# Performance work log

Hardware: AMD Instinct MI355X
Metric: run time of the kernel (lower is better)

The kernel has to match this reference:

```python
import jax, jax.numpy as jnp
import numpy as np

LABEL_SMOOTHING = 0.1
K_SLOPE = 5.0
N, D = 8192, 256


def setup_inputs() -> dict:
    key = jax.random.key(0)
    k1, k2, k3 = jax.random.split(key, 3)
    return {
        "image_features1": jax.random.normal(k1, (N, D), dtype=jnp.float32),
        "image_features2": jax.random.normal(k2, (N, D), dtype=jnp.float32),
        "logit_scale": jnp.asarray(14.2857, dtype=jnp.float32),  # ~ 1/0.07 CLIP temp
        "positive_weights": jax.random.normal(k3, (N,), dtype=jnp.float32),
    }


def _l2_normalize(x, axis=-1, eps=1e-12):
    # matches F.normalize(dim=-1)
    norm = jnp.linalg.norm(x, axis=axis, keepdims=True)
    return x / jnp.maximum(norm, eps)


def _weighted_infonce(sim, eps):
    # per row i: (1-eps_i)*(-sim[i,i] + lse_i) + eps_i*(-mean(sim[i,:]) + lse_i)
    #          = lse_i - (1-eps_i)*sim[i,i] - eps_i*mean_i
    n = sim.shape[0]
    lse = jax.nn.logsumexp(sim, axis=1)            # [n]
    diag = jnp.diagonal(sim)                       # [n]
    row_mean = jnp.mean(sim, axis=1)               # [n]
    per_row = lse - (1.0 - eps) * diag - eps * row_mean
    return jnp.sum(per_row) / n


def reference(image_features1, image_features2, logit_scale, positive_weights):
    f1 = _l2_normalize(image_features1)
    f2 = _l2_normalize(image_features2)
    logits12 = logit_scale * (f1 @ f2.T)           # [N, N]
    # eps = 1 - (1 - label_smoothing) * sigmoid(k * w)
    eps = 1.0 - (1.0 - LABEL_SMOOTHING) * jax.nn.sigmoid(K_SLOPE * positive_weights)
    loss1 = _weighted_infonce(logits12, eps)
    loss2 = _weighted_infonce(logits12.T, eps)
    return (loss1 + loss2) / 2.0
```

## Files before the change

kernel.cpp:

```cpp
#include <hip/hip_runtime.h>
#include <hip/hip_bf16.h>

#define NN 8192
#define DD 256
#define LOG2E 1.4426950408889634f
#define LN2f 0.6931471805599453f

typedef __attribute__((ext_vector_type(8))) short short8;
typedef __attribute__((ext_vector_type(4))) float f32x4;

__device__ __forceinline__ unsigned short f2bf(float x) {
    unsigned int u = __float_as_uint(x);
    u += 0x7fff + ((u >> 16) & 1);
    return (unsigned short)(u >> 16);
}
__device__ __forceinline__ float epsf(float w) {
    return 1.f - 0.9f / (1.f + __expf(-5.f * w));
}

__global__ __launch_bounds__(256) void nrm_kernel(
    const float* __restrict__ f1, const float* __restrict__ f2,
    const float* __restrict__ scale_p, const float* __restrict__ wts,
    unsigned short* __restrict__ f1n, unsigned short* __restrict__ f2n,
    float* __restrict__ diag, float* __restrict__ rse, float* __restrict__ cse,
    float* __restrict__ S1p, float* __restrict__ S2p,
    float* __restrict__ T1p, float* __restrict__ T2p)
{
    __shared__ float4 red[4][256];
    const int w = threadIdx.x >> 6, lane = threadIdx.x & 63;
    const int row = blockIdx.x * 4 + w;
    const float4 a = reinterpret_cast<const float4*>(f1 + (size_t)row * DD)[lane];
    const float4 b = reinterpret_cast<const float4*>(f2 + (size_t)row * DD)[lane];
    float sa = a.x * a.x + a.y * a.y + a.z * a.z + a.w * a.w;
    float sb = b.x * b.x + b.y * b.y + b.z * b.z + b.w * b.w;
    float sab = a.x * b.x + a.y * b.y + a.z * b.z + a.w * b.w;
#pragma unroll
    for (int off = 1; off < 64; off <<= 1) {
        sa += __shfl_xor(sa, off);
        sb += __shfl_xor(sb, off);
        sab += __shfl_xor(sab, off);
    }
    const float s = scale_p[0];
    const float n1 = fmaxf(sqrtf(sa), 1e-12f);
    const float n2 = fmaxf(sqrtf(sb), 1e-12f);
    const float e = epsf(wts[row]);
    if (lane == 0) { diag[row] = s * sab / (n1 * n2); rse[row] = 0.f; cse[row] = 0.f; }
    const float r1 = s * LOG2E / n1, r2 = 1.0f / n2;
    const float v0 = a.x * r1, v1 = a.y * r1, v2 = a.z * r1, v3 = a.w * r1;
    const float u0 = b.x * r2, u1 = b.y * r2, u2 = b.z * r2, u3 = b.w * r2;
    ushort4 o1, o2;
    o1.x = f2bf(v0); o1.y = f2bf(v1); o1.z = f2bf(v2); o1.w = f2bf(v3);
    o2.x = f2bf(u0); o2.y = f2bf(u1); o2.z = f2bf(u2); o2.w = f2bf(u3);
    reinterpret_cast<ushort4*>(f1n + (size_t)row * DD)[lane] = o1;
    reinterpret_cast<ushort4*>(f2n + (size_t)row * DD)[lane] = o2;
    red[w][lane * 4 + 0] = make_float4(v0, e * v0, u0, e * u0);
    red[w][lane * 4 + 1] = make_float4(v1, e * v1, u1, e * u1);
    red[w][lane * 4 + 2] = make_float4(v2, e * v2, u2, e * u2);
    red[w][lane * 4 + 3] = make_float4(v3, e * v3, u3, e * u3);
    __syncthreads();
    const int c = threadIdx.x;
    const int part = (blockIdx.x & 63) * 256 + c;
    const float4 q0 = red[0][c], q1 = red[1][c], q2 = red[2][c], q3 = red[3][c];
    atomicAdd(&S1p[part], q0.x + q1.x + q2.x + q3.x);
    atomicAdd(&T1p[part], q0.y + q1.y + q2.y + q3.y);
    atomicAdd(&S2p[part], q0.z + q1.z + q2.z + q3.z);
    atomicAdd(&T2p[part], q0.w + q1.w + q2.w + q3.w);
}

__global__ __launch_bounds__(256, 2) void gemm_kernel(
    const unsigned short* __restrict__ f1n, const unsigned short* __restrict__ f2n,
    float* __restrict__ rowsumexp, float* __restrict__ colsumexp)
{
    __shared__ char Bs[2][64 * 512];
    __shared__ float colbuf[2][1024];
    const int bid = blockIdx.x;
    const int bm = bid >> 3, bc = bid & 7;
    const int w = threadIdx.x >> 6, lane = threadIdx.x & 63;
    const int wr = (w >> 1) * 64, wc = (w & 1) * 32;
    const int lhi = lane >> 4, llo = lane & 15;

    const char* aBase = (const char*)f1n + ((size_t)(bm * 128 + wr + llo) * 512) + lhi * 16;
    short8 av[4][8];
#pragma unroll
    for (int m = 0; m < 4; ++m)
#pragma unroll
        for (int ks = 0; ks < 8; ++ks)
            av[m][ks] = *(const short8*)(aBase + (size_t)(m * 16) * 512 + ks * 64);
#pragma unroll
    for (int m = 0; m < 4; ++m)
#pragma unroll
        for (int ks = 0; ks < 8; ++ks)
            asm volatile("" : "+v"(av[m][ks]));

    const char* bBase = (const char*)f2n + (size_t)bc * 1024 * 512;

    auto stage = [&](int buf, int tile) {
#pragma unroll
        for (int i = 0; i < 8; ++i) {
            const int r = w * 16 + i * 2 + (lane >> 5);
            const int cs = (lane & 31) ^ (r & 15);
            __builtin_amdgcn_global_load_lds(
                (const __attribute__((address_space(1))) unsigned int*)
                    (bBase + (size_t)(tile * 64 + r) * 512 + cs * 16),
                (__attribute__((address_space(3))) unsigned int*)
                    (&Bs[buf][(w * 16 + i * 2) * 512]), 16, 0, 0);
        }
    };

    float rowpart[16];
#pragma unroll
    for (int i = 0; i < 16; ++i) rowpart[i] = 0.f;

    stage(0, 0);

    const int rb0 = wc + llo, rb1 = wc + 16 + llo;
    const int sw = llo << 4;

    for (int t = 0; t < 16; ++t) {
        const int cur = t & 1;
        if (t < 15) {
            stage(cur ^ 1, t + 1);
            asm volatile("s_waitcnt vmcnt(8)" ::: "memory");
        } else {
            asm volatile("s_waitcnt vmcnt(0)" ::: "memory");
        }
        __builtin_amdgcn_s_barrier();
        __builtin_amdgcn_sched_barrier(0);

        f32x4 acc[4][2];
#pragma unroll
        for (int m = 0; m < 4; ++m) {
            acc[m][0] = (f32x4){0.f, 0.f, 0.f, 0.f};
            acc[m][1] = (f32x4){0.f, 0.f, 0.f, 0.f};
        }
        const char* bs = Bs[cur];
#pragma unroll
        for (int ks = 0; ks < 8; ++ks) {
            const int kb = ks * 64 + lhi * 16;
            const short8 bv0 = *(const short8*)(bs + rb0 * 512 + (kb ^ sw));
            const short8 bv1 = *(const short8*)(bs + rb1 * 512 + (kb ^ sw));
#pragma unroll
            for (int m = 0; m < 4; ++m) {
                acc[m][0] = __builtin_amdgcn_mfma_f32_16x16x32_bf16(av[m][ks], bv0, acc[m][0], 0, 0, 0);
                acc[m][1] = __builtin_amdgcn_mfma_f32_16x16x32_bf16(av[m][ks], bv1, acc[m][1], 0, 0, 0);
            }
        }

        float cee0 = 0.f, cee1 = 0.f;
#pragma unroll
        for (int m = 0; m < 4; ++m)
#pragma unroll
            for (int j = 0; j < 4; ++j) {
                const float e0 = __builtin_exp2f(acc[m][0][j]);
                const float e1 = __builtin_exp2f(acc[m][1][j]);
                rowpart[m * 4 + j] += e0 + e1;
                cee0 += e0; cee1 += e1;
            }
        cee0 += __shfl_xor(cee0, 16); cee0 += __shfl_xor(cee0, 32);
        cee1 += __shfl_xor(cee1, 16); cee1 += __shfl_xor(cee1, 32);
        if (lhi == 0) {
            colbuf[w >> 1][t * 64 + wc + llo] = cee0;
            colbuf[w >> 1][t * 64 + wc + 16 + llo] = cee1;
        }
        __builtin_amdgcn_s_barrier();
    }

    __syncthreads();

#pragma unroll
    for (int m = 0; m < 4; ++m)
#pragma unroll
        for (int j = 0; j < 4; ++j) {
            float v = rowpart[m * 4 + j];
            v += __shfl_xor(v, 1); v += __shfl_xor(v, 2);
            v += __shfl_xor(v, 4); v += __shfl_xor(v, 8);
            if (llo == 0)
                atomicAdd(&rowsumexp[bm * 128 + wr + m * 16 + lhi * 4 + j], v);
        }
    for (int c = threadIdx.x; c < 1024; c += 256)
        atomicAdd(&colsumexp[bc * 1024 + c], colbuf[0][c] + colbuf[1][c]);
}

__global__ __launch_bounds__(256) void finA_kernel(
    const float* __restrict__ rse, const float* __restrict__ cse,
    const float* __restrict__ diag, const float* __restrict__ wts,
    float* __restrict__ totalp)
{
    const int i = blockIdx.x * 256 + threadIdx.x;
    const float eps = epsf(wts[i]);
    float a = __logf(rse[i]) + __logf(cse[i]) - 2.f * (1.f - eps) * diag[i];
#pragma unroll
    for (int off = 1; off < 64; off <<= 1) a += __shfl_xor(a, off);
    __shared__ float red[4];
    if ((threadIdx.x & 63) == 0) red[threadIdx.x >> 6] = a;
    __syncthreads();
    if (threadIdx.x == 0)
        atomicAdd(totalp, red[0] + red[1] + red[2] + red[3]);
}

__global__ __launch_bounds__(1024) void finB_kernel(
    const float* __restrict__ S1p, const float* __restrict__ S2p,
    const float* __restrict__ T1p, const float* __restrict__ T2p,
    const float* __restrict__ totalp, float* __restrict__ out)
{
    const int t = threadIdx.x;
    __shared__ float4 pr4[4][256];
    {
        const int col = t & 255, seg = t >> 8;
        float s1 = 0.f, t1 = 0.f, s2 = 0.f, t2 = 0.f;
#pragma unroll
        for (int q = 0; q < 16; ++q) {
            const int idx = (seg * 16 + q) * 256 + col;
            s1 += S1p[idx]; t1 += T1p[idx]; s2 += S2p[idx]; t2 += T2p[idx];
        }
        pr4[seg][col] = make_float4(s1, t1, s2, t2);
    }
    __syncthreads();
    float a = 0.f;
    if (t < 256) {
        const float4 q0 = pr4[0][t], q1 = pr4[1][t], q2 = pr4[2][t], q3 = pr4[3][t];
        const float s1 = q0.x + q1.x + q2.x + q3.x;
        const float t1 = q0.y + q1.y + q2.y + q3.y;
        const float s2 = q0.z + q1.z + q2.z + q3.z;
        const float t2 = q0.w + q1.w + q2.w + q3.w;
        a = (t1 * s2 + s1 * t2) * (LN2f / (float)NN);
    }
#pragma unroll
    for (int off = 1; off < 64; off <<= 1) a += __shfl_xor(a, off);
    __shared__ float red[16];
    if ((t & 63) == 0) red[t >> 6] = a;
    __syncthreads();
    if (t == 0) {
        float dot = 0.f;
#pragma unroll
        for (int i = 0; i < 16; ++i) dot += red[i];
        out[0] = (totalp[0] - dot) * (1.f / (2.f * (float)NN));
    }
}

extern "C" void kernel_launch(void* const* d_in, const int* in_sizes, int n_in,
                              void* d_out, int out_size, void* d_ws, size_t ws_size,
                              hipStream_t stream) {
    (void)in_sizes; (void)n_in; (void)out_size; (void)ws_size;
    const float* f1 = (const float*)d_in[0];
    const float* f2 = (const float*)d_in[1];
    const float* scale = (const float*)d_in[2];
    const float* wts = (const float*)d_in[3];
    float* out = (float*)d_out;

    char* ws = (char*)d_ws;
    unsigned short* f1n = (unsigned short*)ws;
    unsigned short* f2n = (unsigned short*)(ws + (size_t)4 * 1024 * 1024);
    float* fb = (float*)(ws + (size_t)8 * 1024 * 1024);
    float* rse  = fb;
    float* cse  = fb + 8192;
    float* diag = fb + 16384;
    float* S1p  = fb + 24576;
    float* S2p  = fb + 24576 + 16384;
    float* T1p  = fb + 24576 + 32768;
    float* T2p  = fb + 24576 + 49152;
    float* totalp = fb + 24576 + 65536;

    hipMemsetAsync(S1p, 0, ((size_t)4 * 16384 + 16) * sizeof(float), stream);
    nrm_kernel<<<NN / 4, 256, 0, stream>>>(f1, f2, scale, wts, f1n, f2n,
                                           diag, rse, cse, S1p, S2p, T1p, T2p);
    gemm_kernel<<<512, 256, 0, stream>>>(f1n, f2n, rse, cse);
    finA_kernel<<<32, 256, 0, stream>>>(rse, cse, diag, wts, totalp);
    finB_kernel<<<1, 1024, 0, stream>>>(S1p, S2p, T1p, T2p, totalp, out);
}
```

Measured before the change: 77.08 us.

## Replace atomic column-sum partials with per-block stores and hierarchical reduction

```diff
diff --git a/kernel.cpp b/kernel.cpp
--- a/kernel.cpp
+++ b/kernel.cpp
@@ -23,48 +23,56 @@
     const float* __restrict__ scale_p, const float* __restrict__ wts,
     unsigned short* __restrict__ f1n, unsigned short* __restrict__ f2n,
     float* __restrict__ diag, float* __restrict__ rse, float* __restrict__ cse,
-    float* __restrict__ S1p, float* __restrict__ S2p,
-    float* __restrict__ T1p, float* __restrict__ T2p)
+    float4* __restrict__ STp, float* __restrict__ totalp)
 {
     __shared__ float4 red[4][256];
     const int w = threadIdx.x >> 6, lane = threadIdx.x & 63;
-    const int row = blockIdx.x * 4 + w;
-    const float4 a = reinterpret_cast<const float4*>(f1 + (size_t)row * DD)[lane];
-    const float4 b = reinterpret_cast<const float4*>(f2 + (size_t)row * DD)[lane];
-    float sa = a.x * a.x + a.y * a.y + a.z * a.z + a.w * a.w;
-    float sb = b.x * b.x + b.y * b.y + b.z * b.z + b.w * b.w;
-    float sab = a.x * b.x + a.y * b.y + a.z * b.z + a.w * b.w;
-#pragma unroll
-    for (int off = 1; off < 64; off <<= 1) {
-        sa += __shfl_xor(sa, off);
-        sb += __shfl_xor(sb, off);
-        sab += __shfl_xor(sab, off);
-    }
     const float s = scale_p[0];
-    const float n1 = fmaxf(sqrtf(sa), 1e-12f);
-    const float n2 = fmaxf(sqrtf(sb), 1e-12f);
-    const float e = epsf(wts[row]);
-    if (lane == 0) { diag[row] = s * sab / (n1 * n2); rse[row] = 0.f; cse[row] = 0.f; }
-    const float r1 = s * LOG2E / n1, r2 = 1.0f / n2;
-    const float v0 = a.x * r1, v1 = a.y * r1, v2 = a.z * r1, v3 = a.w * r1;
-    const float u0 = b.x * r2, u1 = b.y * r2, u2 = b.z * r2, u3 = b.w * r2;
-    ushort4 o1, o2;
-    o1.x = f2bf(v0); o1.y = f2bf(v1); o1.z = f2bf(v2); o1.w = f2bf(v3);
-    o2.x = f2bf(u0); o2.y = f2bf(u1); o2.z = f2bf(u2); o2.w = f2bf(u3);
-    reinterpret_cast<ushort4*>(f1n + (size_t)row * DD)[lane] = o1;
-    reinterpret_cast<ushort4*>(f2n + (size_t)row * DD)[lane] = o2;
-    red[w][lane * 4 + 0] = make_float4(v0, e * v0, u0, e * u0);
-    red[w][lane * 4 + 1] = make_float4(v1, e * v1, u1, e * u1);
-    red[w][lane * 4 + 2] = make_float4(v2, e * v2, u2, e * u2);
-    red[w][lane * 4 + 3] = make_float4(v3, e * v3, u3, e * u3);
+    const int row0 = blockIdx.x * 16 + w * 4;
+    float s1a[4] = {0,0,0,0}, t1a[4] = {0,0,0,0};
+    float s2a[4] = {0,0,0,0}, t2a[4] = {0,0,0,0};
+#pragma unroll
+    for (int r = 0; r < 4; ++r) {
+        const int row = row0 + r;
+        const float4 a = reinterpret_cast<const float4*>(f1 + (size_t)row * DD)[lane];
+        const float4 b = reinterpret_cast<const float4*>(f2 + (size_t)row * DD)[lane];
+        float sa = a.x * a.x + a.y * a.y + a.z * a.z + a.w * a.w;
+        float sb = b.x * b.x + b.y * b.y + b.z * b.z + b.w * b.w;
+        float sab = a.x * b.x + a.y * b.y + a.z * b.z + a.w * b.w;
+#pragma unroll
+        for (int off = 1; off < 64; off <<= 1) {
+            sa += __shfl_xor(sa, off);
+            sb += __shfl_xor(sb, off);
+            sab += __shfl_xor(sab, off);
+        }
+        const float n1 = fmaxf(sqrtf(sa), 1e-12f);
+        const float n2 = fmaxf(sqrtf(sb), 1e-12f);
+        const float e = epsf(wts[row]);
+        if (lane == 0) { diag[row] = s * sab / (n1 * n2); rse[row] = 0.f; cse[row] = 0.f; }
+        const float r1 = s * LOG2E / n1, r2 = 1.0f / n2;
+        const float v0 = a.x * r1, v1 = a.y * r1, v2 = a.z * r1, v3 = a.w * r1;
+        const float u0 = b.x * r2, u1 = b.y * r2, u2 = b.z * r2, u3 = b.w * r2;
+        ushort4 o1, o2;
+        o1.x = f2bf(v0); o1.y = f2bf(v1); o1.z = f2bf(v2); o1.w = f2bf(v3);
+        o2.x = f2bf(u0); o2.y = f2bf(u1); o2.z = f2bf(u2); o2.w = f2bf(u3);
+        reinterpret_cast<ushort4*>(f1n + (size_t)row * DD)[lane] = o1;
+        reinterpret_cast<ushort4*>(f2n + (size_t)row * DD)[lane] = o2;
+        s1a[0] += v0; s1a[1] += v1; s1a[2] += v2; s1a[3] += v3;
+        t1a[0] += e * v0; t1a[1] += e * v1; t1a[2] += e * v2; t1a[3] += e * v3;
+        s2a[0] += u0; s2a[1] += u1; s2a[2] += u2; s2a[3] += u3;
+        t2a[0] += e * u0; t2a[1] += e * u1; t2a[2] += e * u2; t2a[3] += e * u3;
+    }
+#pragma unroll
+    for (int k = 0; k < 4; ++k)
+        red[w][lane * 4 + k] = make_float4(s1a[k], t1a[k], s2a[k], t2a[k]);
     __syncthreads();
     const int c = threadIdx.x;
-    const int part = (blockIdx.x & 63) * 256 + c;
     const float4 q0 = red[0][c], q1 = red[1][c], q2 = red[2][c], q3 = red[3][c];
-    atomicAdd(&S1p[part], q0.x + q1.x + q2.x + q3.x);
-    atomicAdd(&T1p[part], q0.y + q1.y + q2.y + q3.y);
-    atomicAdd(&S2p[part], q0.z + q1.z + q2.z + q3.z);
-    atomicAdd(&T2p[part], q0.w + q1.w + q2.w + q3.w);
+    STp[blockIdx.x * 256 + c] = make_float4(q0.x + q1.x + q2.x + q3.x,
+                                            q0.y + q1.y + q2.y + q3.y,
+                                            q0.z + q1.z + q2.z + q3.z,
+                                            q0.w + q1.w + q2.w + q3.w);
+    if (blockIdx.x == 0 && threadIdx.x == 0) totalp[0] = 0.f;
 }
 
 __global__ __launch_bounds__(256, 2) void gemm_kernel(
@@ -184,56 +192,49 @@
 __global__ __launch_bounds__(256) void finA_kernel(
     const float* __restrict__ rse, const float* __restrict__ cse,
     const float* __restrict__ diag, const float* __restrict__ wts,
+    const float4* __restrict__ STp, float4* __restrict__ P2,
     float* __restrict__ totalp)
 {
-    const int i = blockIdx.x * 256 + threadIdx.x;
+    const int g = blockIdx.x, t = threadIdx.x;
+    const int i = g * 256 + t;
     const float eps = epsf(wts[i]);
     float a = __logf(rse[i]) + __logf(cse[i]) - 2.f * (1.f - eps) * diag[i];
 #pragma unroll
     for (int off = 1; off < 64; off <<= 1) a += __shfl_xor(a, off);
     __shared__ float red[4];
-    if ((threadIdx.x & 63) == 0) red[threadIdx.x >> 6] = a;
-    __syncthreads();
-    if (threadIdx.x == 0)
-        atomicAdd(totalp, red[0] + red[1] + red[2] + red[3]);
-}
-
-__global__ __launch_bounds__(1024) void finB_kernel(
-    const float* __restrict__ S1p, const float* __restrict__ S2p,
-    const float* __restrict__ T1p, const float* __restrict__ T2p,
-    const float* __restrict__ totalp, float* __restrict__ out)
+    if ((t & 63) == 0) red[t >> 6] = a;
+
+    float4 s = make_float4(0.f, 0.f, 0.f, 0.f);
+#pragma unroll 4
+    for (int j = 0; j < 16; ++j) {
+        const float4 v = STp[(g * 16 + j) * 256 + t];
+        s.x += v.x; s.y += v.y; s.z += v.z; s.w += v.w;
+    }
+    P2[g * 256 + t] = s;
+
+    __syncthreads();
+    if (t == 0) atomicAdd(totalp, red[0] + red[1] + red[2] + red[3]);
+}
+
+__global__ __launch_bounds__(256) void fin_kernel(
+    const float4* __restrict__ P2, const float* __restrict__ totalp,
+    float* __restrict__ out)
 {
     const int t = threadIdx.x;
-    __shared__ float4 pr4[4][256];
-    {
-        const int col = t & 255, seg = t >> 8;
-        float s1 = 0.f, t1 = 0.f, s2 = 0.f, t2 = 0.f;
-#pragma unroll
-        for (int q = 0; q < 16; ++q) {
-            const int idx = (seg * 16 + q) * 256 + col;
-            s1 += S1p[idx]; t1 += T1p[idx]; s2 += S2p[idx]; t2 += T2p[idx];
-        }
-        pr4[seg][col] = make_float4(s1, t1, s2, t2);
-    }
-    __syncthreads();
-    float a = 0.f;
-    if (t < 256) {
-        const float4 q0 = pr4[0][t], q1 = pr4[1][t], q2 = pr4[2][t], q3 = pr4[3][t];
-        const float s1 = q0.x + q1.x + q2.x + q3.x;
-        const float t1 = q0.y + q1.y + q2.y + q3.y;
-        const float s2 = q0.z + q1.z + q2.z + q3.z;
-        const float t2 = q0.w + q1.w + q2.w + q3.w;
-        a = (t1 * s2 + s1 * t2) * (LN2f / (float)NN);
-    }
-#pragma unroll
-    for (int off = 1; off < 64; off <<= 1) a += __shfl_xor(a, off);
-    __shared__ float red[16];
-    if ((t & 63) == 0) red[t >> 6] = a;
+    float4 s = make_float4(0.f, 0.f, 0.f, 0.f);
+#pragma unroll 4
+    for (int g = 0; g < 32; ++g) {
+        const float4 v = P2[g * 256 + t];
+        s.x += v.x; s.y += v.y; s.z += v.z; s.w += v.w;
+    }
+    float d = (s.y * s.z + s.x * s.w) * (LN2f / (float)NN);
+#pragma unroll
+    for (int off = 1; off < 64; off <<= 1) d += __shfl_xor(d, off);
+    __shared__ float red[4];
+    if ((t & 63) == 0) red[t >> 6] = d;
     __syncthreads();
     if (t == 0) {
-        float dot = 0.f;
-#pragma unroll
-        for (int i = 0; i < 16; ++i) dot += red[i];
+        const float dot = red[0] + red[1] + red[2] + red[3];
         out[0] = (totalp[0] - dot) * (1.f / (2.f * (float)NN));
     }
 }
@@ -252,19 +253,16 @@
     unsigned short* f1n = (unsigned short*)ws;
     unsigned short* f2n = (unsigned short*)(ws + (size_t)4 * 1024 * 1024);
     float* fb = (float*)(ws + (size_t)8 * 1024 * 1024);
-    float* rse  = fb;
-    float* cse  = fb + 8192;
-    float* diag = fb + 16384;
-    float* S1p  = fb + 24576;
-    float* S2p  = fb + 24576 + 16384;
-    float* T1p  = fb + 24576 + 32768;
-    float* T2p  = fb + 24576 + 49152;
-    float* totalp = fb + 24576 + 65536;
-
-    hipMemsetAsync(S1p, 0, ((size_t)4 * 16384 + 16) * sizeof(float), stream);
-    nrm_kernel<<<NN / 4, 256, 0, stream>>>(f1, f2, scale, wts, f1n, f2n,
-                                           diag, rse, cse, S1p, S2p, T1p, T2p);
+    float* rse    = fb;
+    float* cse    = fb + 8192;
+    float* diag   = fb + 16384;
+    float* totalp = fb + 24576;
+    float4* STp   = (float4*)(fb + 32768);
+    float4* P2    = (float4*)(fb + 32768 + 524288);
+
+    nrm_kernel<<<512, 256, 0, stream>>>(f1, f2, scale, wts, f1n, f2n,
+                                        diag, rse, cse, STp, totalp);
     gemm_kernel<<<512, 256, 0, stream>>>(f1n, f2n, rse, cse);
-    finA_kernel<<<32, 256, 0, stream>>>(rse, cse, diag, wts, totalp);
-    finB_kernel<<<1, 1024, 0, stream>>>(S1p, S2p, T1p, T2p, totalp, out);
-}
+    finA_kernel<<<32, 256, 0, stream>>>(rse, cse, diag, wts, STp, P2, totalp);
+    fin_kernel<<<1, 256, 0, stream>>>(P2, totalp, out);
+}
```

Measured after the change: 70.15 us. -9.0%, faster.
